# Performance work log

Hardware: AMD Instinct MI355X
Metric: run time of the kernel (lower is better)

Reference implementation:

```python
import jax, jax.numpy as jnp
import numpy as np

B, P, CIN, PS = 8192, 9, 12, 64   # batch, patches, channels, patch_size
D_IN = CIN * PS                    # 768 flattened patch features
ENC_H, D = 512, 1024               # patch_encoder_hidden, embedding_dim
E, EXP_H, C = 8, 2048, 1000        # num_experts, expert hidden, num_classes
SYM, SYM_H = 6, 64                 # symbolic_dim, symbolic gating hidden


def setup_inputs() -> dict:
    key = jax.random.key(0)
    ks = jax.random.split(key, 16)
    g = lambda k, shape, fan: jax.random.normal(k, shape, jnp.float32) / np.sqrt(fan)
    return {
        "patches": jax.random.normal(ks[0], (B, P, CIN, PS), jnp.float32),
        "symbolic_features": jax.random.normal(ks[1], (B, SYM), jnp.float32),
        # patch encoder (2-layer MLP per patch)
        "enc_w1": g(ks[2], (D_IN, ENC_H), D_IN), "enc_b1": jnp.zeros((ENC_H,), jnp.float32),
        "enc_w2": g(ks[3], (ENC_H, D), ENC_H),   "enc_b2": jnp.zeros((D,), jnp.float32),
        # neural gating: Linear(D,D)-ReLU-Linear(D,E)
        "gn_w1": g(ks[4], (D, D), D), "gn_b1": jnp.zeros((D,), jnp.float32),
        "gn_w2": g(ks[5], (D, E), D), "gn_b2": jnp.zeros((E,), jnp.float32),
        # symbolic gating: Linear(SYM,64)-ReLU-Linear(64,E)
        "gs_w1": g(ks[6], (SYM, SYM_H), SYM),  "gs_b1": jnp.zeros((SYM_H,), jnp.float32),
        "gs_w2": g(ks[7], (SYM_H, E), SYM_H),  "gs_b2": jnp.zeros((E,), jnp.float32),
        # stacked experts: Linear(D,H)-ReLU-(Dropout=eval identity)-Linear(H,C)
        "ew1": g(ks[8], (E, D, EXP_H), D),      "eb1": jnp.zeros((E, EXP_H), jnp.float32),
        "ew2": g(ks[9], (E, EXP_H, C), EXP_H),  "eb2": jnp.zeros((E, C), jnp.float32),
    }


def reference(patches, symbolic_features, enc_w1, enc_b1, enc_w2, enc_b2,
              gn_w1, gn_b1, gn_w2, gn_b2, gs_w1, gs_b1, gs_w2, gs_b2,
              ew1, eb1, ew2, eb2):
    b = patches.shape[0]
    # patch encoder: (b, P, CIN*PS) -> (b, P, D)
    x = patches.reshape(b, P, D_IN)
    h = jax.nn.relu(jnp.einsum('bpf,fh->bph', x, enc_w1) + enc_b1)
    encoded = jnp.einsum('bph,hd->bpd', h, enc_w2) + enc_b2
    # mean aggregation over patches
    agg = encoded.mean(axis=1)  # (b, D)
    # symbolic gating: 0.5*neural + 0.5*symbolic logits, softmax
    neural = jax.nn.relu(agg @ gn_w1 + gn_b1) @ gn_w2 + gn_b2            # (b, E)
    symb = jax.nn.relu(symbolic_features @ gs_w1 + gs_b1) @ gs_w2 + gs_b2  # (b, E)
    gating_weights = jax.nn.softmax(0.5 * neural + 0.5 * symb, axis=1)
    # all experts densely (batched over expert axis)
    eh = jax.nn.relu(jnp.einsum('bd,edh->beh', agg, ew1) + eb1)          # (b, E, H)
    expert_logits = jnp.einsum('beh,ehc->bec', eh, ew2) + eb2            # (b, E, C)
    # gate-weighted sum
    logits = jnp.einsum('be,bec->bc', gating_weights, expert_logits)     # (b, C)
    return logits, gating_weights, expert_logits
```

## Files before the change

kernel.cpp:

```cpp
#include <hip/hip_runtime.h>
#include <hip/hip_bf16.h>

typedef __attribute__((ext_vector_type(8))) short s16x8;
typedef __attribute__((ext_vector_type(4))) float f32x4;

#define DEV __device__ __forceinline__

DEV short f2b(float f) {
  __hip_bfloat16 h = __float2bfloat16(f);
  short s; __builtin_memcpy(&s, &h, 2); return s;
}
DEV float b2f(short s) {
  __hip_bfloat16 h; __builtin_memcpy(&h, &s, 2); return __bfloat162float(h);
}

typedef __attribute__((address_space(1))) const void gvoid;
typedef __attribute__((address_space(3))) void lvoid;
DEV void gload_lds16(const void* g, void* l) {
  __builtin_amdgcn_global_load_lds((gvoid*)g, (lvoid*)l, 16, 0, 0);
}

static constexpr int kB = 8192, kP = 9, kDIN = 768, kENCH = 512, kD = 1024;
static constexpr int kE = 8, kH = 2048, kC = 1000;
static constexpr size_t OUT_GATE   = (size_t)kB * kC;
static constexpr size_t OUT_EL     = OUT_GATE + (size_t)kB * kE;

static constexpr size_t W1T  = 0;
static constexpr size_t W2T  = W1T  + 786432;
static constexpr size_t GW1T = W2T  + 1048576;
static constexpr size_t EW1T = GW1T + 2097152;
static constexpr size_t EW2T = EW1T + 33554432;
static constexpr size_t PBF  = EW2T + 32768000;
static constexpr size_t HBUF = PBF  + 113246208;
static constexpr size_t EH4  = HBUF + 75497472;
static constexpr size_t HMEAN = PBF;
static constexpr size_t AGG   = HMEAN + 8388608;
static constexpr size_t GH    = AGG   + 16777216;
static constexpr size_t NEU   = GH    + 16777216;
static constexpr size_t SYMB  = NEU   + 262144;

__global__ void cast_bf16_kernel(const float* __restrict__ in, short* __restrict__ out, size_t n8) {
  size_t i = (size_t)blockIdx.x * blockDim.x + threadIdx.x;
  if (i >= n8) return;
  float4 a = ((const float4*)in)[i * 2];
  float4 b = ((const float4*)in)[i * 2 + 1];
  s16x8 v;
  v[0] = f2b(a.x); v[1] = f2b(a.y); v[2] = f2b(a.z); v[3] = f2b(a.w);
  v[4] = f2b(b.x); v[5] = f2b(b.y); v[6] = f2b(b.z); v[7] = f2b(b.w);
  *(s16x8*)(out + i * 8) = v;
}

__global__ void transpose_cast_kernel(const float* __restrict__ in, short* __restrict__ out,
                                      int R, int C, size_t istride, size_t ostride) {
  __shared__ float tile[32][33];
  const float* W = in + istride * blockIdx.z;
  short* T = out + ostride * blockIdx.z;
  int tx = threadIdx.x, ty = threadIdx.y;
  int c0 = blockIdx.x * 32, r0 = blockIdx.y * 32;
  #pragma unroll
  for (int i = 0; i < 32; i += 8) {
    int r = r0 + ty + i, c = c0 + tx;
    if (r < R && c < C) tile[ty + i][tx] = W[(size_t)r * C + c];
  }
  __syncthreads();
  #pragma unroll
  for (int i = 0; i < 32; i += 8) {
    int rr = c0 + ty + i, cc = r0 + tx;
    if (rr < C && cc < R) T[(size_t)rr * R + cc] = f2b(tile[tx][ty + i]);
  }
}

#define BARR() __builtin_amdgcn_s_barrier()
#define VMW6() asm volatile("s_waitcnt vmcnt(6)" ::: "memory")
#define VMW4() asm volatile("s_waitcnt vmcnt(4)" ::: "memory")
#define VMW0() asm volatile("s_waitcnt vmcnt(0)" ::: "memory")

template<bool RELU, bool F32OUT, bool NTAIL>
__global__ __launch_bounds__(512, 2)
void gemm256_kernel(const short* __restrict__ A, const short* __restrict__ Bt,
                    const float* __restrict__ bias, void* __restrict__ Cout,
                    int M, int N, int K, int ldc,
                    long aZ, long bZ, long biasZ, long cZ) {
  __shared__ short Abuf[2][2][8192];
  __shared__ short Bbuf[2][2][8192];
  const int z = blockIdx.z;
  A += (size_t)z * aZ; Bt += (size_t)z * bZ; bias += (size_t)z * biasZ;

  const int XT = gridDim.x;
  int lid = blockIdx.y * XT + blockIdx.x;
  const int cpx = (XT * gridDim.y) >> 3;
  lid = (lid & 7) * cpx + (lid >> 3);
  const int bx = lid % XT, by = lid / XT;
  const int bM = by * 256, bN = bx * 256;

  const int t = threadIdx.x, lane = t & 63, wid = t >> 6;
  const int wm = wid & 1, wn = wid >> 1;
  const int lr = lane & 15, kg = lane >> 4;
  const int nkt = K >> 6;

  const int srB = t >> 3;
  const int sx = (t & 7) ^ (srB & 7);
  const int ldsoff = wid * 512;

  int br0 = bN + srB, br1 = bN + 64 + srB, br2 = bN + 128 + srB, br3 = bN + 192 + srB;
  if (NTAIL) {
    if (br0 >= N) br0 = N - 1;
    if (br1 >= N) br1 = N - 1;
    if (br2 >= N) br2 = N - 1;
    if (br3 >= N) br3 = N - 1;
  }
  const short* pA00 = A + (size_t)(bM + srB) * K + sx * 8;
  const short* pA01 = A + (size_t)(bM + 64 + srB) * K + sx * 8;
  const short* pA10 = A + (size_t)(bM + 128 + srB) * K + sx * 8;
  const short* pA11 = A + (size_t)(bM + 192 + srB) * K + sx * 8;
  const short* pB00 = Bt + (size_t)br0 * K + sx * 8;
  const short* pB01 = Bt + (size_t)br1 * K + sx * 8;
  const short* pB10 = Bt + (size_t)br2 * K + sx * 8;
  const short* pB11 = Bt + (size_t)br3 * K + sx * 8;

#define STAGE_A0(tile_) do { if ((tile_) < nkt) { int par_ = (tile_) & 1; \
    gload_lds16(pA00, &Abuf[par_][0][ldsoff]); \
    gload_lds16(pA01, &Abuf[par_][0][4096 + ldsoff]); \
    pA00 += 64; pA01 += 64; } } while (0)
#define STAGE_A1(tile_) do { if ((tile_) < nkt) { int par_ = (tile_) & 1; \
    gload_lds16(pA10, &Abuf[par_][1][ldsoff]); \
    gload_lds16(pA11, &Abuf[par_][1][4096 + ldsoff]); \
    pA10 += 64; pA11 += 64; } } while (0)
#define STAGE_B0(tile_) do { if ((tile_) < nkt) { int par_ = (tile_) & 1; \
    gload_lds16(pB00, &Bbuf[par_][0][ldsoff]); \
    gload_lds16(pB01, &Bbuf[par_][0][4096 + ldsoff]); \
    pB00 += 64; pB01 += 64; } } while (0)
#define STAGE_B1(tile_) do { if ((tile_) < nkt) { int par_ = (tile_) & 1; \
    gload_lds16(pB10, &Bbuf[par_][1][ldsoff]); \
    gload_lds16(pB11, &Bbuf[par_][1][4096 + ldsoff]); \
    pB10 += 64; pB11 += 64; } } while (0)

  const int aro = (wm * 64 + lr) * 64;
  const int bro = (wn * 32 + lr) * 64;
  const int so0 = (kg ^ (lr & 7)) * 8;
  const int so1 = ((4 + kg) ^ (lr & 7)) * 8;

  s16x8 a0[4][2], a1[4][2], b0[2][2], b1[2][2];
#define LDA0(par_) do { _Pragma("unroll") \
    for (int m_ = 0; m_ < 4; ++m_) { \
      a0[m_][0] = *(const s16x8*)&Abuf[par_][0][aro + m_ * 1024 + so0]; \
      a0[m_][1] = *(const s16x8*)&Abuf[par_][0][aro + m_ * 1024 + so1]; \
    } } while (0)
#define LDA1(par_) do { _Pragma("unroll") \
    for (int m_ = 0; m_ < 4; ++m_) { \
      a1[m_][0] = *(const s16x8*)&Abuf[par_][1][aro + m_ * 1024 + so0]; \
      a1[m_][1] = *(const s16x8*)&Abuf[par_][1][aro + m_ * 1024 + so1]; \
    } } while (0)
#define LDB0(par_) do { _Pragma("unroll") \
    for (int n_ = 0; n_ < 2; ++n_) { \
      b0[n_][0] = *(const s16x8*)&Bbuf[par_][0][bro + n_ * 1024 + so0]; \
      b0[n_][1] = *(const s16x8*)&Bbuf[par_][0][bro + n_ * 1024 + so1]; \
    } } while (0)
#define LDB1(par_) do { _Pragma("unroll") \
    for (int n_ = 0; n_ < 2; ++n_) { \
      b1[n_][0] = *(const s16x8*)&Bbuf[par_][1][bro + n_ * 1024 + so0]; \
      b1[n_][1] = *(const s16x8*)&Bbuf[par_][1][bro + n_ * 1024 + so1]; \
    } } while (0)

  f32x4 acc[2][2][4][2];
  #pragma unroll
  for (int a_ = 0; a_ < 2; ++a_)
    #pragma unroll
    for (int b_ = 0; b_ < 2; ++b_)
      #pragma unroll
      for (int m_ = 0; m_ < 4; ++m_)
        #pragma unroll
        for (int n_ = 0; n_ < 2; ++n_) acc[a_][b_][m_][n_] = (f32x4){0.f, 0.f, 0.f, 0.f};

#define MMAQ(mh, nh, AF, BF) do { \
    __builtin_amdgcn_s_setprio(1); \
    _Pragma("unroll") \
    for (int m_ = 0; m_ < 4; ++m_) \
      _Pragma("unroll") \
      for (int n_ = 0; n_ < 2; ++n_) { \
        acc[mh][nh][m_][n_] = __builtin_amdgcn_mfma_f32_16x16x32_bf16(AF[m_][0], BF[n_][0], acc[mh][nh][m_][n_], 0, 0, 0); \
        acc[mh][nh][m_][n_] = __builtin_amdgcn_mfma_f32_16x16x32_bf16(AF[m_][1], BF[n_][1], acc[mh][nh][m_][n_], 0, 0, 0); \
      } \
    __builtin_amdgcn_s_setprio(0); } while (0)

  STAGE_A0(0); STAGE_B0(0); STAGE_B1(0); STAGE_A1(0);
  VMW4();
  STAGE_A0(1); STAGE_B0(1); STAGE_B1(1);
  VMW6();
  BARR();

  for (int g = 0; g < nkt; ++g) {
    const int par = g & 1;
    LDA0(par); LDB0(par); LDB1(par);
    STAGE_A1(g + 1);
    MMAQ(0, 0, a0, b0);
    MMAQ(0, 1, a0, b1);
    BARR();
    LDA1(par);
    STAGE_A0(g + 2); STAGE_B0(g + 2); STAGE_B1(g + 2);
    MMAQ(1, 1, a1, b1);
    MMAQ(1, 0, a1, b0);
    if (g == nkt - 2) { VMW0(); } else if (g < nkt - 2) { VMW6(); }
    BARR();
  }

  #pragma unroll
  for (int nh = 0; nh < 2; ++nh)
    #pragma unroll
    for (int n_ = 0; n_ < 2; ++n_) {
      int col = bN + nh * 128 + wn * 32 + n_ * 16 + lr;
      if (NTAIL && col >= N) continue;
      float bv = bias[col];
      #pragma unroll
      for (int mh = 0; mh < 2; ++mh)
        #pragma unroll
        for (int m_ = 0; m_ < 4; ++m_) {
          int row0 = bM + mh * 128 + wm * 64 + m_ * 16 + kg * 4;
          #pragma unroll
          for (int r_ = 0; r_ < 4; ++r_) {
            float v = acc[mh][nh][m_][n_][r_] + bv;
            if (RELU) v = fmaxf(v, 0.f);
            size_t off = (size_t)(row0 + r_) * ldc + col;
            if (F32OUT) ((float*)Cout + (size_t)z * cZ)[off] = v;
            else        ((short*)Cout + (size_t)z * cZ)[off] = f2b(v);
          }
        }
    }
#undef STAGE_A0
#undef STAGE_A1
#undef STAGE_B0
#undef STAGE_B1
#undef LDA0
#undef LDA1
#undef LDB0
#undef LDB1
#undef MMAQ
}

__global__ void mean9_kernel(const short* __restrict__ h, short* __restrict__ hm) {
  size_t i = (size_t)blockIdx.x * blockDim.x + threadIdx.x;
  if (i >= (size_t)kB * kENCH / 8) return;
  size_t b = i >> 6; int d8 = (int)(i & 63);
  const short* base = h + b * kP * kENCH + d8 * 8;
  float s[8] = {0, 0, 0, 0, 0, 0, 0, 0};
  #pragma unroll
  for (int p = 0; p < kP; ++p) {
    s16x8 v = *(const s16x8*)(base + p * kENCH);
    #pragma unroll
    for (int j = 0; j < 8; ++j) s[j] += b2f(v[j]);
  }
  s16x8 o;
  #pragma unroll
  for (int j = 0; j < 8; ++j) o[j] = f2b(s[j] * (1.f / 9.f));
  *(s16x8*)(hm + i * 8) = o;
}

__global__ __launch_bounds__(256)
void gating_neural_kernel(const short* __restrict__ gh, const float* __restrict__ w2,
                          const float* __restrict__ b2, float* __restrict__ neural) {
  int wid = threadIdx.x >> 6, lane = threadIdx.x & 63;
  int row = blockIdx.x * 4 + wid;
  float acc[8] = {0,0,0,0,0,0,0,0};
  const short* grow = gh + (size_t)row * kD;
  for (int k = lane; k < kD; k += 64) {
    float x = b2f(grow[k]);
    const float* w = w2 + (size_t)k * 8;
    #pragma unroll
    for (int c = 0; c < 8; ++c) acc[c] += x * w[c];
  }
  #pragma unroll
  for (int c = 0; c < 8; ++c)
    #pragma unroll
    for (int off = 32; off >= 1; off >>= 1) acc[c] += __shfl_xor(acc[c], off);
  if (lane == 0) {
    #pragma unroll
    for (int c = 0; c < 8; ++c) neural[(size_t)row * 8 + c] = acc[c] + b2[c];
  }
}

__global__ __launch_bounds__(256)
void gating_symb_kernel(const float* __restrict__ sym, const float* __restrict__ w1,
                        const float* __restrict__ b1, const float* __restrict__ w2,
                        const float* __restrict__ b2, float* __restrict__ symb) {
  int wid = threadIdx.x >> 6, lane = threadIdx.x & 63;
  int row = blockIdx.x * 4 + wid;
  float s0 = sym[(size_t)row * 6 + 0], s1 = sym[(size_t)row * 6 + 1], s2 = sym[(size_t)row * 6 + 2];
  float s3 = sym[(size_t)row * 6 + 3], s4 = sym[(size_t)row * 6 + 4], s5 = sym[(size_t)row * 6 + 5];
  float hh = b1[lane];
  hh += s0 * w1[0 * 64 + lane] + s1 * w1[1 * 64 + lane] + s2 * w1[2 * 64 + lane];
  hh += s3 * w1[3 * 64 + lane] + s4 * w1[4 * 64 + lane] + s5 * w1[5 * 64 + lane];
  hh = fmaxf(hh, 0.f);
  float acc[8];
  #pragma unroll
  for (int c = 0; c < 8; ++c) acc[c] = hh * w2[lane * 8 + c];
  #pragma unroll
  for (int c = 0; c < 8; ++c)
    #pragma unroll
    for (int off = 32; off >= 1; off >>= 1) acc[c] += __shfl_xor(acc[c], off);
  if (lane == 0) {
    #pragma unroll
    for (int c = 0; c < 8; ++c) symb[(size_t)row * 8 + c] = acc[c] + b2[c];
  }
}

__global__ void gating_softmax_kernel(const float* __restrict__ neural, const float* __restrict__ symb,
                                      float* __restrict__ gate_out) {
  int row = blockIdx.x * blockDim.x + threadIdx.x;
  if (row >= kB) return;
  float g[8], m = -1e30f;
  #pragma unroll
  for (int c = 0; c < 8; ++c) {
    g[c] = 0.5f * (neural[(size_t)row * 8 + c] + symb[(size_t)row * 8 + c]);
    m = fmaxf(m, g[c]);
  }
  float sum = 0.f;
  #pragma unroll
  for (int c = 0; c < 8; ++c) { g[c] = expf(g[c] - m); sum += g[c]; }
  float inv = 1.f / sum;
  #pragma unroll
  for (int c = 0; c < 8; ++c) gate_out[(size_t)row * 8 + c] = g[c] * inv;
}

__global__ __launch_bounds__(256)
void combine_kernel(float* __restrict__ out) {
  int b = blockIdx.y;
  int c = blockIdx.x * 256 + threadIdx.x;
  __shared__ float g[8];
  if (threadIdx.x < 8) g[threadIdx.x] = out[OUT_GATE + (size_t)b * 8 + threadIdx.x];
  __syncthreads();
  if (c < kC) {
    const float* el = out + OUT_EL + (size_t)b * (kE * kC) + c;
    float a = 0.f;
    #pragma unroll
    for (int e = 0; e < 8; ++e) a += g[e] * el[e * kC];
    out[(size_t)b * kC + c] = a;
  }
}

extern "C" void kernel_launch(void* const* d_in, const int* in_sizes, int n_in,
                              void* d_out, int out_size, void* d_ws, size_t ws_size,
                              hipStream_t stream) {
  const float* patches = (const float*)d_in[0];
  const float* symf    = (const float*)d_in[1];
  const float* enc_w1  = (const float*)d_in[2];
  const float* enc_b1  = (const float*)d_in[3];
  const float* enc_w2  = (const float*)d_in[4];
  const float* enc_b2  = (const float*)d_in[5];
  const float* gn_w1   = (const float*)d_in[6];
  const float* gn_b1   = (const float*)d_in[7];
  const float* gn_w2   = (const float*)d_in[8];
  const float* gn_b2   = (const float*)d_in[9];
  const float* gs_w1   = (const float*)d_in[10];
  const float* gs_b1   = (const float*)d_in[11];
  const float* gs_w2   = (const float*)d_in[12];
  const float* gs_b2   = (const float*)d_in[13];
  const float* ew1     = (const float*)d_in[14];
  const float* eb1     = (const float*)d_in[15];
  const float* ew2     = (const float*)d_in[16];
  const float* eb2     = (const float*)d_in[17];
  char* ws = (char*)d_ws;
  float* out = (float*)d_out;
  dim3 tb(32, 8);

  {
    size_t n8 = (size_t)kB * kP * kDIN / 8;
    cast_bf16_kernel<<<(unsigned)((n8 + 255) / 256), 256, 0, stream>>>(patches, (short*)(ws + PBF), n8);
  }
  transpose_cast_kernel<<<dim3(16, 24, 1), tb, 0, stream>>>(enc_w1, (short*)(ws + W1T),  kDIN,  kENCH, 0, 0);
  transpose_cast_kernel<<<dim3(32, 16, 1), tb, 0, stream>>>(enc_w2, (short*)(ws + W2T),  kENCH, kD,    0, 0);
  transpose_cast_kernel<<<dim3(32, 32, 1), tb, 0, stream>>>(gn_w1,  (short*)(ws + GW1T), kD,    kD,    0, 0);
  transpose_cast_kernel<<<dim3(64, 32, 8), tb, 0, stream>>>(ew1,    (short*)(ws + EW1T), kD,    kH,
                                                            (size_t)kD * kH, (size_t)kD * kH);
  transpose_cast_kernel<<<dim3(32, 64, 8), tb, 0, stream>>>(ew2,    (short*)(ws + EW2T), kH,    kC,
                                                            (size_t)kH * kC, (size_t)kH * kC);
  gemm256_kernel<true, false, false><<<dim3(2, 288, 1), 512, 0, stream>>>(
      (short*)(ws + PBF), (short*)(ws + W1T), enc_b1, ws + HBUF,
      kB * kP, kENCH, kDIN, kENCH, 0, 0, 0, 0);
  mean9_kernel<<<(kB * kENCH / 8) / 256, 256, 0, stream>>>((short*)(ws + HBUF), (short*)(ws + HMEAN));
  gemm256_kernel<false, false, false><<<dim3(4, 32, 1), 512, 0, stream>>>(
      (short*)(ws + HMEAN), (short*)(ws + W2T), enc_b2, ws + AGG,
      kB, kD, kENCH, kD, 0, 0, 0, 0);
  gemm256_kernel<true, false, false><<<dim3(4, 32, 1), 512, 0, stream>>>(
      (short*)(ws + AGG), (short*)(ws + GW1T), gn_b1, ws + GH,
      kB, kD, kD, kD, 0, 0, 0, 0);
  gating_neural_kernel<<<kB / 4, 256, 0, stream>>>((short*)(ws + GH), gn_w2, gn_b2, (float*)(ws + NEU));
  gating_symb_kernel<<<kB / 4, 256, 0, stream>>>(symf, gs_w1, gs_b1, gs_w2, gs_b2, (float*)(ws + SYMB));
  gating_softmax_kernel<<<kB / 256, 256, 0, stream>>>((float*)(ws + NEU), (float*)(ws + SYMB), out + OUT_GATE);
  for (int h = 0; h < 2; ++h) {
    int e0 = h * 4;
    gemm256_kernel<true, false, false><<<dim3(8, 32, 4), 512, 0, stream>>>(
        (short*)(ws + AGG), (short*)(ws + EW1T) + (size_t)e0 * kH * kD, eb1 + (size_t)e0 * kH,
        ws + EH4, kB, kH, kD, kH,
        0, (long)kH * kD, kH, (long)kB * kH);
    gemm256_kernel<false, true, true><<<dim3(4, 32, 4), 512, 0, stream>>>(
        (short*)(ws + EH4), (short*)(ws + EW2T) + (size_t)e0 * kC * kH, eb2 + (size_t)e0 * kC,
        out + OUT_EL + (size_t)e0 * kC, kB, kC, kH, kE * kC,
        (long)kB * kH, (long)kC * kH, kC, kC);
  }
  combine_kernel<<<dim3(4, kB), 256, 0, stream>>>(out);
}
```

Before: 974.4 us.

## Add 128-row GEMM variant, fuse gating kernels, launch all experts at once

Adds a gemm128 kernel with 128x256 tiles and higher occupancy for the two small 8192x1024 GEMMs so that more blocks fill the GPU. Fuses the neural gating projection, the symbolic gating MLP and the softmax into one kernel, which removes two launches and the intermediate buffers. When the workspace is large enough, the expert GEMMs run as single launches over all 8 experts instead of two halves, which needs a larger expert-hidden buffer. The new GEMM uses a simpler double buffer with a full vmcnt(0) wait each iteration, which may expose memory latency.

```diff
diff --git a/kernel.cpp b/kernel.cpp
--- a/kernel.cpp
+++ b/kernel.cpp
@@ -33,11 +33,10 @@
 static constexpr size_t PBF  = EW2T + 32768000;
 static constexpr size_t HBUF = PBF  + 113246208;
 static constexpr size_t EH4  = HBUF + 75497472;
+static constexpr size_t WS_Z8 = EH4 + (size_t)8 * kB * kH * 2;
 static constexpr size_t HMEAN = PBF;
 static constexpr size_t AGG   = HMEAN + 8388608;
 static constexpr size_t GH    = AGG   + 16777216;
-static constexpr size_t NEU   = GH    + 16777216;
-static constexpr size_t SYMB  = NEU   + 262144;
 
 __global__ void cast_bf16_kernel(const float* __restrict__ in, short* __restrict__ out, size_t n8) {
   size_t i = (size_t)blockIdx.x * blockDim.x + threadIdx.x;
@@ -73,6 +72,7 @@
 #define BARR() __builtin_amdgcn_s_barrier()
 #define VMW6() asm volatile("s_waitcnt vmcnt(6)" ::: "memory")
 #define VMW4() asm volatile("s_waitcnt vmcnt(4)" ::: "memory")
+#define VMW3() asm volatile("s_waitcnt vmcnt(3)" ::: "memory")
 #define VMW0() asm volatile("s_waitcnt vmcnt(0)" ::: "memory")
 
 template<bool RELU, bool F32OUT, bool NTAIL>
@@ -237,6 +237,115 @@
 #undef MMAQ
 }
 
+template<bool RELU, bool F32OUT, bool NTAIL>
+__global__ __launch_bounds__(512, 4)
+void gemm128_kernel(const short* __restrict__ A, const short* __restrict__ Bt,
+                    const float* __restrict__ bias, void* __restrict__ Cout,
+                    int M, int N, int K, int ldc,
+                    long aZ, long bZ, long biasZ, long cZ) {
+  __shared__ short Abuf[2][4096];
+  __shared__ short Bbuf[2][2][4096];
+  const int z = blockIdx.z;
+  A += (size_t)z * aZ; Bt += (size_t)z * bZ; bias += (size_t)z * biasZ;
+
+  const int XT = gridDim.x;
+  int lid = blockIdx.y * XT + blockIdx.x;
+  const int cpx = (XT * gridDim.y) >> 3;
+  lid = (lid & 7) * cpx + (lid >> 3);
+  const int bx = lid % XT, by = lid / XT;
+  const int bM = by * 128, bN = bx * 256;
+
+  const int t = threadIdx.x, lane = t & 63, wid = t >> 6;
+  const int wm = wid & 1, wn = wid >> 1;
+  const int lr = lane & 15, kg = lane >> 4;
+  const int nkt = K >> 5;
+
+  const int srB = t >> 2;
+  const int sx = (t & 3) ^ ((srB >> 1) & 3);
+  const int ldsoff = wid * 512;
+
+  int br0 = bN + srB, br1 = bN + 128 + srB;
+  if (NTAIL) {
+    if (br0 >= N) br0 = N - 1;
+    if (br1 >= N) br1 = N - 1;
+  }
+  const short* pA  = A + (size_t)(bM + srB) * K + sx * 8;
+  const short* pB0 = Bt + (size_t)br0 * K + sx * 8;
+  const short* pB1 = Bt + (size_t)br1 * K + sx * 8;
+
+#define STAGE(tile_) do { if ((tile_) < nkt) { int par_ = (tile_) & 1; \
+    gload_lds16(pA,  &Abuf[par_][ldsoff]); \
+    gload_lds16(pB0, &Bbuf[par_][0][ldsoff]); \
+    gload_lds16(pB1, &Bbuf[par_][1][ldsoff]); \
+    pA += 32; pB0 += 32; pB1 += 32; } } while (0)
+
+  const int aro = (wm * 64 + lr) * 32;
+  const int bro = (wn * 32 + lr) * 32;
+  const int so = (kg ^ ((lr >> 1) & 3)) * 8;
+
+  s16x8 a[4], b0[2], b1[2];
+#define LDFRAGS(par_) do { \
+    _Pragma("unroll") \
+    for (int m_ = 0; m_ < 4; ++m_) a[m_] = *(const s16x8*)&Abuf[par_][aro + m_ * 512 + so]; \
+    _Pragma("unroll") \
+    for (int n_ = 0; n_ < 2; ++n_) { \
+      b0[n_] = *(const s16x8*)&Bbuf[par_][0][bro + n_ * 512 + so]; \
+      b1[n_] = *(const s16x8*)&Bbuf[par_][1][bro + n_ * 512 + so]; \
+    } } while (0)
+
+  f32x4 acc[2][4][2];
+  #pragma unroll
+  for (int h_ = 0; h_ < 2; ++h_)
+    #pragma unroll
+    for (int m_ = 0; m_ < 4; ++m_)
+      #pragma unroll
+      for (int n_ = 0; n_ < 2; ++n_) acc[h_][m_][n_] = (f32x4){0.f, 0.f, 0.f, 0.f};
+
+  STAGE(0);
+  VMW0();
+  BARR();
+
+  for (int g = 0; g < nkt; ++g) {
+    const int par = g & 1;
+    LDFRAGS(par);
+    STAGE(g + 1);
+    __builtin_amdgcn_s_setprio(1);
+    #pragma unroll
+    for (int m_ = 0; m_ < 4; ++m_)
+      #pragma unroll
+      for (int n_ = 0; n_ < 2; ++n_) {
+        acc[0][m_][n_] = __builtin_amdgcn_mfma_f32_16x16x32_bf16(a[m_], b0[n_], acc[0][m_][n_], 0, 0, 0);
+        acc[1][m_][n_] = __builtin_amdgcn_mfma_f32_16x16x32_bf16(a[m_], b1[n_], acc[1][m_][n_], 0, 0, 0);
+      }
+    __builtin_amdgcn_s_setprio(0);
+    VMW0();
+    BARR();
+  }
+
+  #pragma unroll
+  for (int nh = 0; nh < 2; ++nh)
+    #pragma unroll
+    for (int n_ = 0; n_ < 2; ++n_) {
+      int col = bN + nh * 128 + wn * 32 + n_ * 16 + lr;
+      if (NTAIL && col >= N) continue;
+      float bv = bias[col];
+      #pragma unroll
+      for (int m_ = 0; m_ < 4; ++m_) {
+        int row0 = bM + wm * 64 + m_ * 16 + kg * 4;
+        #pragma unroll
+        for (int r_ = 0; r_ < 4; ++r_) {
+          float v = acc[nh][m_][n_][r_] + bv;
+          if (RELU) v = fmaxf(v, 0.f);
+          size_t off = (size_t)(row0 + r_) * ldc + col;
+          if (F32OUT) ((float*)Cout + (size_t)z * cZ)[off] = v;
+          else        ((short*)Cout + (size_t)z * cZ)[off] = f2b(v);
+        }
+      }
+    }
+#undef STAGE
+#undef LDFRAGS
+}
+
 __global__ void mean9_kernel(const short* __restrict__ h, short* __restrict__ hm) {
   size_t i = (size_t)blockIdx.x * blockDim.x + threadIdx.x;
   if (i >= (size_t)kB * kENCH / 8) return;
@@ -256,69 +365,52 @@
 }
 
 __global__ __launch_bounds__(256)
-void gating_neural_kernel(const short* __restrict__ gh, const float* __restrict__ w2,
-                          const float* __restrict__ b2, float* __restrict__ neural) {
+void gating_fused_kernel(const short* __restrict__ gh,
+                         const float* __restrict__ gn_w2, const float* __restrict__ gn_b2,
+                         const float* __restrict__ sym,
+                         const float* __restrict__ gs_w1, const float* __restrict__ gs_b1,
+                         const float* __restrict__ gs_w2, const float* __restrict__ gs_b2,
+                         float* __restrict__ gate_out) {
   int wid = threadIdx.x >> 6, lane = threadIdx.x & 63;
   int row = blockIdx.x * 4 + wid;
   float acc[8] = {0,0,0,0,0,0,0,0};
   const short* grow = gh + (size_t)row * kD;
   for (int k = lane; k < kD; k += 64) {
     float x = b2f(grow[k]);
-    const float* w = w2 + (size_t)k * 8;
+    const float* w = gn_w2 + (size_t)k * 8;
     #pragma unroll
     for (int c = 0; c < 8; ++c) acc[c] += x * w[c];
   }
-  #pragma unroll
-  for (int c = 0; c < 8; ++c)
-    #pragma unroll
-    for (int off = 32; off >= 1; off >>= 1) acc[c] += __shfl_xor(acc[c], off);
-  if (lane == 0) {
-    #pragma unroll
-    for (int c = 0; c < 8; ++c) neural[(size_t)row * 8 + c] = acc[c] + b2[c];
-  }
-}
-
-__global__ __launch_bounds__(256)
-void gating_symb_kernel(const float* __restrict__ sym, const float* __restrict__ w1,
-                        const float* __restrict__ b1, const float* __restrict__ w2,
-                        const float* __restrict__ b2, float* __restrict__ symb) {
-  int wid = threadIdx.x >> 6, lane = threadIdx.x & 63;
-  int row = blockIdx.x * 4 + wid;
   float s0 = sym[(size_t)row * 6 + 0], s1 = sym[(size_t)row * 6 + 1], s2 = sym[(size_t)row * 6 + 2];
   float s3 = sym[(size_t)row * 6 + 3], s4 = sym[(size_t)row * 6 + 4], s5 = sym[(size_t)row * 6 + 5];
-  float hh = b1[lane];
-  hh += s0 * w1[0 * 64 + lane] + s1 * w1[1 * 64 + lane] + s2 * w1[2 * 64 + lane];
-  hh += s3 * w1[3 * 64 + lane] + s4 * w1[4 * 64 + lane] + s5 * w1[5 * 64 + lane];
+  float hh = gs_b1[lane];
+  hh += s0 * gs_w1[0 * 64 + lane] + s1 * gs_w1[1 * 64 + lane] + s2 * gs_w1[2 * 64 + lane];
+  hh += s3 * gs_w1[3 * 64 + lane] + s4 * gs_w1[4 * 64 + lane] + s5 * gs_w1[5 * 64 + lane];
   hh = fmaxf(hh, 0.f);
-  float acc[8];
-  #pragma unroll
-  for (int c = 0; c < 8; ++c) acc[c] = hh * w2[lane * 8 + c];
+  float acc2[8];
+  #pragma unroll
+  for (int c = 0; c < 8; ++c) acc2[c] = hh * gs_w2[lane * 8 + c];
   #pragma unroll
   for (int c = 0; c < 8; ++c)
     #pragma unroll
-    for (int off = 32; off >= 1; off >>= 1) acc[c] += __shfl_xor(acc[c], off);
+    for (int off = 32; off >= 1; off >>= 1) {
+      acc[c]  += __shfl_xor(acc[c], off);
+      acc2[c] += __shfl_xor(acc2[c], off);
+    }
   if (lane == 0) {
-    #pragma unroll
-    for (int c = 0; c < 8; ++c) symb[(size_t)row * 8 + c] = acc[c] + b2[c];
-  }
-}
-
-__global__ void gating_softmax_kernel(const float* __restrict__ neural, const float* __restrict__ symb,
-                                      float* __restrict__ gate_out) {
-  int row = blockIdx.x * blockDim.x + threadIdx.x;
-  if (row >= kB) return;
-  float g[8], m = -1e30f;
-  #pragma unroll
-  for (int c = 0; c < 8; ++c) {
-    g[c] = 0.5f * (neural[(size_t)row * 8 + c] + symb[(size_t)row * 8 + c]);
-    m = fmaxf(m, g[c]);
-  }
-  float sum = 0.f;
-  #pragma unroll
-  for (int c = 0; c < 8; ++c) { g[c] = expf(g[c] - m); sum += g[c]; }
-  float inv = 1.f / sum;
-  #pragma unroll
-  for (int c = 0; c < 8; ++c) gate_out[(size_t)row * 8 + c] = g[c] * inv;
+    float g[8], m = -1e30f;
+    #pragma unroll
+    for (int c = 0; c < 8; ++c) {
+      g[c] = 0.5f * ((acc[c] + gn_b2[c]) + (acc2[c] + gs_b2[c]));
+      m = fmaxf(m, g[c]);
+    }
+    float sum = 0.f;
+    #pragma unroll
+    for (int c = 0; c < 8; ++c) { g[c] = expf(g[c] - m); sum += g[c]; }
+    float inv = 1.f / sum;
+    #pragma unroll
+    for (int c = 0; c < 8; ++c) gate_out[(size_t)row * 8 + c] = g[c] * inv;
+  }
 }
 
 __global__ __launch_bounds__(256)
@@ -377,25 +469,35 @@
       (short*)(ws + PBF), (short*)(ws + W1T), enc_b1, ws + HBUF,
       kB * kP, kENCH, kDIN, kENCH, 0, 0, 0, 0);
   mean9_kernel<<<(kB * kENCH / 8) / 256, 256, 0, stream>>>((short*)(ws + HBUF), (short*)(ws + HMEAN));
-  gemm256_kernel<false, false, false><<<dim3(4, 32, 1), 512, 0, stream>>>(
+  gemm128_kernel<false, false, false><<<dim3(4, 64, 1), 512, 0, stream>>>(
       (short*)(ws + HMEAN), (short*)(ws + W2T), enc_b2, ws + AGG,
       kB, kD, kENCH, kD, 0, 0, 0, 0);
-  gemm256_kernel<true, false, false><<<dim3(4, 32, 1), 512, 0, stream>>>(
+  gemm128_kernel<true, false, false><<<dim3(4, 64, 1), 512, 0, stream>>>(
       (short*)(ws + AGG), (short*)(ws + GW1T), gn_b1, ws + GH,
       kB, kD, kD, kD, 0, 0, 0, 0);
-  gating_neural_kernel<<<kB / 4, 256, 0, stream>>>((short*)(ws + GH), gn_w2, gn_b2, (float*)(ws + NEU));
-  gating_symb_kernel<<<kB / 4, 256, 0, stream>>>(symf, gs_w1, gs_b1, gs_w2, gs_b2, (float*)(ws + SYMB));
-  gating_softmax_kernel<<<kB / 256, 256, 0, stream>>>((float*)(ws + NEU), (float*)(ws + SYMB), out + OUT_GATE);
-  for (int h = 0; h < 2; ++h) {
-    int e0 = h * 4;
-    gemm256_kernel<true, false, false><<<dim3(8, 32, 4), 512, 0, stream>>>(
-        (short*)(ws + AGG), (short*)(ws + EW1T) + (size_t)e0 * kH * kD, eb1 + (size_t)e0 * kH,
+  gating_fused_kernel<<<kB / 4, 256, 0, stream>>>(
+      (short*)(ws + GH), gn_w2, gn_b2, symf, gs_w1, gs_b1, gs_w2, gs_b2, out + OUT_GATE);
+  if (ws_size >= WS_Z8) {
+    gemm256_kernel<true, false, false><<<dim3(8, 32, 8), 512, 0, stream>>>(
+        (short*)(ws + AGG), (short*)(ws + EW1T), eb1,
         ws + EH4, kB, kH, kD, kH,
         0, (long)kH * kD, kH, (long)kB * kH);
-    gemm256_kernel<false, true, true><<<dim3(4, 32, 4), 512, 0, stream>>>(
-        (short*)(ws + EH4), (short*)(ws + EW2T) + (size_t)e0 * kC * kH, eb2 + (size_t)e0 * kC,
-        out + OUT_EL + (size_t)e0 * kC, kB, kC, kH, kE * kC,
+    gemm256_kernel<false, true, true><<<dim3(4, 32, 8), 512, 0, stream>>>(
+        (short*)(ws + EH4), (short*)(ws + EW2T), eb2,
+        out + OUT_EL, kB, kC, kH, kE * kC,
         (long)kB * kH, (long)kC * kH, kC, kC);
+  } else {
+    for (int h = 0; h < 2; ++h) {
+      int e0 = h * 4;
+      gemm256_kernel<true, false, false><<<dim3(8, 32, 4), 512, 0, stream>>>(
+          (short*)(ws + AGG), (short*)(ws + EW1T) + (size_t)e0 * kH * kD, eb1 + (size_t)e0 * kH,
+          ws + EH4, kB, kH, kD, kH,
+          0, (long)kH * kD, kH, (long)kB * kH);
+      gemm256_kernel<false, true, true><<<dim3(4, 32, 4), 512, 0, stream>>>(
+          (short*)(ws + EH4), (short*)(ws + EW2T) + (size_t)e0 * kC * kH, eb2 + (size_t)e0 * kC,
+          out + OUT_EL + (size_t)e0 * kC, kB, kC, kH, kE * kC,
+          (long)kB * kH, (long)kC * kH, kC, kC);
+    }
   }
   combine_kernel<<<dim3(4, kB), 256, 0, stream>>>(out);
 }
```

Result: no change. 961.1 us (-1.4%).
